# Optimization experiments

Measured on AMD Instinct MI355X. Metric: run time of the kernel, lower is better.

Reference implementation:

```python
import jax, jax.numpy as jnp
import numpy as np

NUM_NODES = 127   # complete binary tree of depth 7: parent(i) = (i-1)//2
BATCH = 262144
DEPTH = 7


def _project(p):
    """DAG min-propagation in topological order, vectorized per tree level.

    Equivalent to: for parent in topo_order: for child in children(parent):
        p[:, child] = min(p[:, child], p[:, parent])
    Each child has exactly one parent, and parents are always processed before
    children when sweeping levels top-down, so level-parallel updates match the
    edge-sequential reference exactly.
    """
    for level in range(1, DEPTH):
        start, end = 2 ** level - 1, 2 ** (level + 1) - 1
        idx = jnp.arange(start, end)          # children at this level
        par = (idx - 1) // 2                  # their unique parents
        p = p.at[:, idx].set(jnp.minimum(p[:, idx], p[:, par]))
    return p


def setup_inputs() -> dict:
    key = jax.random.key(0)
    x = jax.random.normal(key, (BATCH, NUM_NODES), dtype=jnp.float32)
    return {"x": x}


def reference(x):
    # DAGConstraintLayer.forward: sigmoid then hard DAG projection
    return _project(jax.nn.sigmoid(x))
```

## Files before the change

kernel.cpp:

```cpp
#include <hip/hip_runtime.h>


#define NODES 127
#define RPB   32
#define BLOCK 256
#define TILE_F4 (RPB * NODES / 4)

__device__ __forceinline__ float sigf(float v) {
    return 1.0f / (1.0f + __expf(-v));
}

template<int D>
__device__ __forceinline__ void visit(float* __restrict__ buf, int o, int n, float pm) {
    float v = fminf(pm, buf[o + n]);
    buf[o + n] = sigf(v);
    if constexpr (D > 1) {
        visit<D - 1>(buf, o, 2 * n + 1, v);
        visit<D - 1>(buf, o, 2 * n + 2, v);
    }
}

__global__ __launch_bounds__(BLOCK, 8) void dag_kernel(const float* __restrict__ x,
                                                       float* __restrict__ out) {
    __shared__ float buf[RPB * NODES];

    const size_t base = (size_t)blockIdx.x * (RPB * NODES);

    const float4* __restrict__ src = (const float4*)(x + base);
    float4* __restrict__ b4 = (float4*)buf;
    int t = threadIdx.x;
    #pragma unroll
    for (int k = 0; k < 3; ++k) b4[t + k * BLOCK] = src[t + k * BLOCK];
    if (t + 3 * BLOCK < TILE_F4) b4[t + 3 * BLOCK] = src[t + 3 * BLOCK];
    __syncthreads();

    const int rl = t >> 3;
    const int s  = t & 7;
    const int o  = rl * NODES;
    const int m3 = 7 + s;
    const int m2 = (m3 - 1) >> 1;
    const int m1 = (m2 - 1) >> 1;

    float x0 = buf[o];
    float a1 = buf[o + m1];
    float a2 = buf[o + m2];

    if (s == 0) {
        float X2 = buf[o + 2], X4 = buf[o + 4];
        float X5 = buf[o + 5], X6 = buf[o + 6];
        float p1 = fminf(x0, a1);
        float p2 = fminf(x0, X2);
        buf[o + 0] = sigf(x0);
        buf[o + 1] = sigf(p1);
        buf[o + 2] = sigf(p2);
        buf[o + 3] = sigf(fminf(p1, a2));
        buf[o + 4] = sigf(fminf(p1, X4));
        buf[o + 5] = sigf(fminf(p2, X5));
        buf[o + 6] = sigf(fminf(p2, X6));
    }

    float pm = fminf(fminf(x0, a1), a2);
    visit<4>(buf, o, m3, pm);
    __syncthreads();

    float4* __restrict__ dst = (float4*)(out + base);
    #pragma unroll
    for (int k = 0; k < 3; ++k) dst[t + k * BLOCK] = b4[t + k * BLOCK];
    if (t + 3 * BLOCK < TILE_F4) dst[t + 3 * BLOCK] = b4[t + 3 * BLOCK];
}

extern "C" void kernel_launch(void* const* d_in, const int* in_sizes, int n_in,
                              void* d_out, int out_size, void* d_ws, size_t ws_size,
                              hipStream_t stream) {
    const float* x = (const float*)d_in[0];
    float* out = (float*)d_out;
    int rows = in_sizes[0] / NODES;
    int grid = rows / RPB;
    dag_kernel<<<grid, BLOCK, 0, stream>>>(x, out);
}
```

Measured before the change: 229.3 us.

## Map one tree row per wavefront and propagate minima with cross-lane permutes

New measurement: 238.9 us. +4.2%, slower.

```diff
diff --git a/kernel.cpp b/kernel.cpp
--- a/kernel.cpp
+++ b/kernel.cpp
@@ -2,71 +2,67 @@
 
 
 #define NODES 127
-#define RPB   32
 #define BLOCK 256
-#define TILE_F4 (RPB * NODES / 4)
+#define WPB   (BLOCK / 64)
+#define TPW   32
 
 __device__ __forceinline__ float sigf(float v) {
     return 1.0f / (1.0f + __expf(-v));
 }
 
-template<int D>
-__device__ __forceinline__ void visit(float* __restrict__ buf, int o, int n, float pm) {
-    float v = fminf(pm, buf[o + n]);
-    buf[o + n] = sigf(v);
-    if constexpr (D > 1) {
-        visit<D - 1>(buf, o, 2 * n + 1, v);
-        visit<D - 1>(buf, o, 2 * n + 2, v);
-    }
+__device__ __forceinline__ float bperm_min(float p, int idx) {
+    return fminf(p, __int_as_float(
+        __builtin_amdgcn_ds_bpermute(idx, __float_as_int(p))));
 }
 
 __global__ __launch_bounds__(BLOCK, 8) void dag_kernel(const float* __restrict__ x,
                                                        float* __restrict__ out) {
-    __shared__ float buf[RPB * NODES];
+    const int t  = threadIdx.x;
+    const int wv = t >> 6;
+    const int l  = t & 63;
+    const long long W    = (long long)blockIdx.x * WPB + wv;
+    const long long row0 = W * TPW;
 
-    const size_t base = (size_t)blockIdx.x * (RPB * NODES);
+    const int i1 = ((l + 1) >> 1) - 1;
+    const int i2 = ((l + 1) >> 2) - 1;
+    const int i4 = ((l + 1) >> 4) - 1;
+    const int s1 = 4 * (i1 < 0 ? 0 : i1);
+    const int s2 = 4 * (i2 < 0 ? 0 : i2);
+    const int s4 = 4 * (i4 < 0 ? 0 : i4);
+    const int sB = 4 * ((63 + l) >> 1);
+    const int lb = (l < 63) ? l : 62;
 
-    const float4* __restrict__ src = (const float4*)(x + base);
-    float4* __restrict__ b4 = (float4*)buf;
-    int t = threadIdx.x;
+    const float* __restrict__ xp = x   + row0 * NODES;
+    float*       __restrict__ op = out + row0 * NODES;
+
+    float A[4], B[4];
+
+#define LOADROW(j, slot) do {                                   \
+        const float* rp_ = xp + (size_t)(j) * NODES;            \
+        A[slot] = rp_[l];                                       \
+        B[slot] = rp_[64 + lb];                                 \
+    } while (0)
+
+    LOADROW(0, 0);
+    LOADROW(1, 1);
+
     #pragma unroll
-    for (int k = 0; k < 3; ++k) b4[t + k * BLOCK] = src[t + k * BLOCK];
-    if (t + 3 * BLOCK < TILE_F4) b4[t + 3 * BLOCK] = src[t + 3 * BLOCK];
-    __syncthreads();
+    for (int j = 0; j < TPW; ++j) {
+        const int cs = j & 3;
+        if (j + 2 < TPW) LOADROW(j + 2, (j + 2) & 3);
 
-    const int rl = t >> 3;
-    const int s  = t & 7;
-    const int o  = rl * NODES;
-    const int m3 = 7 + s;
-    const int m2 = (m3 - 1) >> 1;
-    const int m1 = (m2 - 1) >> 1;
+        float p = A[cs];
+        p = bperm_min(p, s1);
+        p = bperm_min(p, s2);
+        p = bperm_min(p, s4);
+        float q = fminf(B[cs], __int_as_float(
+            __builtin_amdgcn_ds_bpermute(sB, __float_as_int(p))));
 
-    float x0 = buf[o];
-    float a1 = buf[o + m1];
-    float a2 = buf[o + m2];
-
-    if (s == 0) {
-        float X2 = buf[o + 2], X4 = buf[o + 4];
-        float X5 = buf[o + 5], X6 = buf[o + 6];
-        float p1 = fminf(x0, a1);
-        float p2 = fminf(x0, X2);
-        buf[o + 0] = sigf(x0);
-        buf[o + 1] = sigf(p1);
-        buf[o + 2] = sigf(p2);
-        buf[o + 3] = sigf(fminf(p1, a2));
-        buf[o + 4] = sigf(fminf(p1, X4));
-        buf[o + 5] = sigf(fminf(p2, X5));
-        buf[o + 6] = sigf(fminf(p2, X6));
+        float* rp = op + (size_t)j * NODES;
+        rp[l] = sigf(p);
+        if (l < 63) rp[64 + l] = sigf(q);
     }
-
-    float pm = fminf(fminf(x0, a1), a2);
-    visit<4>(buf, o, m3, pm);
-    __syncthreads();
-
-    float4* __restrict__ dst = (float4*)(out + base);
-    #pragma unroll
-    for (int k = 0; k < 3; ++k) dst[t + k * BLOCK] = b4[t + k * BLOCK];
-    if (t + 3 * BLOCK < TILE_F4) dst[t + 3 * BLOCK] = b4[t + 3 * BLOCK];
+#undef LOADROW
 }
 
 extern "C" void kernel_launch(void* const* d_in, const int* in_sizes, int n_in,
@@ -74,7 +70,8 @@
                               hipStream_t stream) {
     const float* x = (const float*)d_in[0];
     float* out = (float*)d_out;
-    int rows = in_sizes[0] / NODES;
-    int grid = rows / RPB;
+    int rows  = in_sizes[0] / NODES;
+    int waves = rows / TPW;
+    int grid  = waves / WPB;
     dag_kernel<<<grid, BLOCK, 0, stream>>>(x, out);
 }
```
